# Kernel tuning notes

Measured on AMD Instinct MI355X. Metric: run time of the kernel, lower is better.

## Reference

```python
import jax, jax.numpy as jnp
import numpy as np
from jax import lax

S, B, K, T = 16, 16, 3, 20
FP, DP = 64, 28
CP = FP - DP + 1            # 37
P = CP * CP                 # 1369 == num_pixels
H, Hh, D = 256, 128, 2


def setup_inputs() -> dict:
    key = jax.random.key(0)
    ks = jax.random.split(key, 20)

    def lin_w(k, fan_in, fan_out):
        return jax.random.normal(k, (fan_in, fan_out), jnp.float32) / np.sqrt(fan_in)

    inp = {
        "frames": jax.random.uniform(ks[0], (B, T, FP, FP), jnp.float32),
        "digit": jax.random.uniform(ks[1], (S, B, K, DP, DP), jnp.float32),
        # enc_hidden: Linear(P, H)
        "w_h1": lin_w(ks[2], P, H), "b_h1": jnp.zeros((H,), jnp.float32),
        # where_mean: Linear(H, Hh) -> ReLU -> Linear(Hh, D) -> Tanh
        "wm1": lin_w(ks[3], H, Hh), "bm1": jnp.zeros((Hh,), jnp.float32),
        "wm2": lin_w(ks[4], Hh, D), "bm2": jnp.zeros((D,), jnp.float32),
        # where_log_std: Linear(H, Hh) -> ReLU -> Linear(Hh, D)
        "ws1": lin_w(ks[5], H, Hh), "bs1": jnp.zeros((Hh,), jnp.float32),
        "ws2": lin_w(ks[6], Hh, D), "bs2": jnp.zeros((D,), jnp.float32),
        # disp_mean: Linear(P, H) -> ReLU -> Linear(H, Hh) -> ReLU -> Linear(Hh, D) -> Tanh
        "wd1": lin_w(ks[7], P, H), "bd1": jnp.zeros((H,), jnp.float32),
        "wd2": lin_w(ks[8], H, Hh), "bd2": jnp.zeros((Hh,), jnp.float32),
        "wd3": lin_w(ks[9], Hh, D), "bd3": jnp.zeros((D,), jnp.float32),
    }
    return inp


def _lin(x, w, b):
    return x @ w + b


def _forward(frames, digit, w_h1, b_h1, wm1, bm1, wm2, bm2,
             ws1, bs1, ws2, bs2, wd1, bd1, wd2, bd2, wd3, bd3):
    # frames: (B, T, FP, FP); digit: (S, B, K, DP, DP)
    s, b, k_ = digit.shape[0], digit.shape[1], digit.shape[2]
    t = frames.shape[1]

    # Template correlation. The original builds a (T, S*B*K, FP, FP) repeated
    # input and runs conv2d with groups=S*B*K. Since frames do not depend on
    # (s, k), the identical math is a grouped conv with groups=B where group b
    # holds the S*K templates for batch element b.
    x = frames.transpose(1, 0, 2, 3)                          # (T, B, FP, FP)
    kern = digit.transpose(1, 0, 2, 3, 4).reshape(b * s * k_, 1, DP, DP)
    conv = lax.conv_general_dilated(
        x, kern, window_strides=(1, 1), padding='VALID',
        dimension_numbers=('NCHW', 'OIHW', 'NCHW'),
        feature_group_count=b)                                # (T, B*S*K, CP, CP)
    cp = conv.shape[-1]
    conv = conv.reshape(t, b, s, k_, cp * cp)
    conv = conv.transpose(2, 1, 0, 3, 4)                      # (S, B, T, K, P)

    # temporal displacement of correlation maps
    conv_disp = conv[:, :, 1:] - conv[:, :, :-1]              # (S, B, T-1, K, P)

    # disp_mean MLP
    d = jax.nn.relu(_lin(conv_disp, wd1, bd1))
    d = jax.nn.relu(_lin(d, wd2, bd2))
    disp = jnp.tanh(_lin(d, wd3, bd3))                        # (S, B, T-1, K, D)

    # enc_hidden on softmax-normalized correlation maps
    hidden = jax.nn.relu(_lin(jax.nn.softmax(conv, axis=-1), w_h1, b_h1))

    q_mean = jnp.tanh(_lin(jax.nn.relu(_lin(hidden, wm1, bm1)), wm2, bm2))
    q_std = jnp.exp(_lin(jax.nn.relu(_lin(hidden, ws1, bs1)), ws2, bs2))
    return q_mean, q_std, disp


def reference(frames, digit, w_h1, b_h1, wm1, bm1, wm2, bm2,
              ws1, bs1, ws2, bs2, wd1, bd1, wd2, bd2, wd3, bd3):
    return _forward(frames, digit, w_h1, b_h1, wm1, bm1, wm2, bm2,
                    ws1, bs1, ws2, bs2, wd1, bd1, wd2, bd2, wd3, bd3)
```

## Files before the change

### kernel.cpp

```cpp
#include <hip/hip_runtime.h>
#include <hip/hip_fp16.h>

typedef __attribute__((ext_vector_type(8))) _Float16 half8;
typedef __attribute__((ext_vector_type(2))) _Float16 h2f;
typedef __attribute__((ext_vector_type(4))) float f32x4;

#define NP 1369
#define KP 1376
#define NKT 43
#define ROWS_A 15360
#define ROWS_D 14592

#define PA_OFF   0
#define PD_OFF   (ROWS_A * KP)
#define PWH_OFF  (PD_OFF + ROWS_D * KP)
#define PWD_OFF  (PWH_OFF + NKT * 16 * 512)
#define PW2_OFF  (PWD_OFF + NKT * 16 * 512)
#define PWD2_OFF (PW2_OFF + 8 * 16 * 512)
#define TSUM_OFF (PWD2_OFF + 8 * 8 * 512)

#define SHIFT_DW 2384

__device__ __forceinline__ unsigned short f2h(float f) {
    __half h = __float2half(f);
    return __half_as_ushort(h);
}
__device__ __forceinline__ h2f u2h2(unsigned int u) {
    h2f r; __builtin_memcpy(&r, &u, 4); return r;
}

__global__ __launch_bounds__(256)
void k0_pack(const float* __restrict__ w_h1, const float* __restrict__ wd1,
             const float* __restrict__ wm1,  const float* __restrict__ ws1,
             const float* __restrict__ wd2,  const float* __restrict__ digit,
             unsigned short* __restrict__ wsu, float* __restrict__ tsum)
{
    const int tid = threadIdx.x;
    if (blockIdx.x >= 3136) {
        const int sbk = (blockIdx.x - 3136) * 4 + (tid >> 6);
        const int l = tid & 63;
        const float* tp = digit + (size_t)sbk * 784;
        float s = 0.f;
        for (int i = l; i < 784; i += 64) s += tp[i];
        for (int o = 32; o; o >>= 1) s += __shfl_xor(s, o, 64);
        if (l == 0) tsum[sbk] = 0.5f * s;
        return;
    }
    int idx = blockIdx.x * 256 + tid;
    int local, mode;
    unsigned short* dst;
    if (idx < 352256)      { mode = 0; local = idx;          dst = wsu + PWH_OFF; }
    else if (idx < 704512) { mode = 1; local = idx - 352256; dst = wsu + PWD_OFF; }
    else if (idx < 770048) { mode = 2; local = idx - 704512; dst = wsu + PW2_OFF; }
    else                   { mode = 3; local = idx - 770048; dst = wsu + PWD2_OFF; }
    int j = local & 7, lane = (local >> 3) & 63, rest = local >> 9;
    int NTn = (mode == 3) ? 8 : 16;
    int nt = rest % NTn, kt = rest / NTn;
    int k = kt * 32 + ((lane >> 4) << 3) + j;
    int n = nt * 16 + (lane & 15);
    float v = 0.f;
    if (mode == 0)      { if (k < NP) v = w_h1[k * 256 + n]; }
    else if (mode == 1) { if (k < NP) v = wd1[k * 256 + n]; }
    else if (mode == 2) { v = (n < 128) ? wm1[k * 128 + n] : ws1[k * 128 + (n - 128)]; }
    else                { v = wd2[k * 128 + n]; }
    dst[local] = f2h(v);
}

__global__ __launch_bounds__(512)
void k1a_corr(const float* __restrict__ frames, const float* __restrict__ digit,
              const float* __restrict__ tsum, unsigned short* __restrict__ wsu)
{
    __shared__ __align__(16) unsigned short Bs[7 * 3 * 512];
    __shared__ __align__(16) unsigned int frd[SHIFT_DW + 64 * 37];
    __shared__ float Cn[48];

    const int tid = threadIdx.x, l = tid & 63, w = tid >> 6;
    const int mh = blockIdx.x & 1;
    const int bt = blockIdx.x >> 1;
    const int t  = bt % 20;
    const int bb = bt / 20;

    if (tid < 48) {
        int sbk_n = ((tid / 3) * 16 + bb) * 3 + (tid % 3);
        Cn[tid] = tsum[sbk_n];
    }
    if (tid < 320) {
        int r = tid / 5, d2 = tid - r * 5;
        frd[r * 37 + 32 + d2] = 0u;
        frd[SHIFT_DW + r * 37 + 32 + d2] = 0u;
    }
    {
        const float4* fp4 = (const float4*)(frames + (size_t)(bb * 20 + t) * 4096);
        for (int idx = tid; idx < 1024; idx += 512) {
            float4 v = fp4[idx];
            int r = idx >> 4, c4 = idx & 15;
            unsigned lo = (unsigned)f2h(v.x) | ((unsigned)f2h(v.y) << 16);
            unsigned hi = (unsigned)f2h(v.z) | ((unsigned)f2h(v.w) << 16);
            frd[r * 37 + c4 * 2]     = lo;
            frd[r * 37 + c4 * 2 + 1] = hi;
        }
    }
    __syncthreads();
    for (int i = tid; i < 64 * 34; i += 512) {
        int r = i / 34, d = i - r * 34;
        unsigned lo = frd[r * 37 + d], hi = frd[r * 37 + d + 1];
        frd[SHIFT_DW + r * 37 + d] = (lo >> 16) | (hi << 16);
    }

    const int c15 = l & 15, quad = l >> 4, v0q = quad << 3;
    const int cnt = (50 - w) / 8;

    int baseb[6];
#pragma unroll
    for (int it = 0; it < 6; ++it) {
        int tI = mh * 43 + w + 8 * it;
        int p  = tI * 16 + c15;
        int pc = p > 1368 ? 1368 : p;
        int i  = pc / 37;
        int jj = pc - i * 37;
        int c  = jj + v0q;
        baseb[it] = (c & 1) * (SHIFT_DW * 4) + i * 148 + ((c >> 1) << 2);
    }
    f32x4 acc[6][3];
#pragma unroll
    for (int it = 0; it < 6; ++it)
#pragma unroll
        for (int nt = 0; nt < 3; ++nt) acc[it][nt] = (f32x4){0.f, 0.f, 0.f, 0.f};

    for (int ph = 0; ph < 4; ++ph) {
        __syncthreads();
        for (int s = tid; s < 1344; s += 512) {
            int ktl = s / 192;
            int rem = s - ktl * 192;
            int nt = rem >> 6, sl = rem & 63;
            int nl = nt * 16 + (sl & 15);
            int v0 = (sl >> 4) << 3;
            int kt = ph * 7 + ktl;
            int sbk_n = ((nl / 3) * 16 + bb) * 3 + (nl % 3);
            const float* tp = digit + (size_t)sbk_n * 784 + kt * 28 + v0;
            float4 fa = *(const float4*)tp;
            float4 fb = (v0 <= 16) ? *(const float4*)(tp + 4) : make_float4(0.f, 0.f, 0.f, 0.f);
            uint4 pk;
            pk.x = (unsigned)f2h(fa.x) | ((unsigned)f2h(fa.y) << 16);
            pk.y = (unsigned)f2h(fa.z) | ((unsigned)f2h(fa.w) << 16);
            pk.z = (unsigned)f2h(fb.x) | ((unsigned)f2h(fb.y) << 16);
            pk.w = (unsigned)f2h(fb.z) | ((unsigned)f2h(fb.w) << 16);
            *(uint4*)(Bs + s * 8) = pk;
        }
        __syncthreads();

        for (int ktl = 0; ktl < 7; ++ktl) {
            const int kt = ph * 7 + ktl;
            half8 bf0 = *(const half8*)(Bs + ktl * 1536 + 0 * 512 + l * 8);
            half8 bf1 = *(const half8*)(Bs + ktl * 1536 + 1 * 512 + l * 8);
            half8 bf2 = *(const half8*)(Bs + ktl * 1536 + 2 * 512 + l * 8);
            const char* fb2 = (const char*)frd + (size_t)kt * 148;
#pragma unroll
            for (int it = 0; it < 6; ++it) {
                if (it < cnt) {
                    const unsigned* ap = (const unsigned*)(fb2 + baseb[it]);
                    union { unsigned u[4]; half8 h8; } af;
                    af.u[0] = ap[0];
                    af.u[1] = ap[1];
                    af.u[2] = ap[2];
                    af.u[3] = ap[3];
                    acc[it][0] = __builtin_amdgcn_mfma_f32_16x16x32_f16(af.h8, bf0, acc[it][0], 0, 0, 0);
                    acc[it][1] = __builtin_amdgcn_mfma_f32_16x16x32_f16(af.h8, bf1, acc[it][1], 0, 0, 0);
                    acc[it][2] = __builtin_amdgcn_mfma_f32_16x16x32_f16(af.h8, bf2, acc[it][2], 0, 0, 0);
                }
            }
        }
    }

    for (int itg = 0; itg < 6; ++itg) {
        __syncthreads();
        if (itg < cnt) {
#pragma unroll
            for (int nt = 0; nt < 3; ++nt) {
                const int nl = nt * 16 + c15;
                const float C = Cn[nl];
                ushort4 st;
                st.x = f2h(acc[itg][nt][0] - C);
                st.y = f2h(acc[itg][nt][1] - C);
                st.z = f2h(acc[itg][nt][2] - C);
                st.w = f2h(acc[itg][nt][3] - C);
                *(ushort4*)(Bs + nl * 136 + w * 16 + quad * 4) = st;
            }
        }
        __syncthreads();
        const int nseg = (itg == 5) ? 6 : 16;
        for (int i = tid; i < 48 * nseg; i += 512) {
            int rowl = i / nseg, seg = i - rowl * nseg;
            int sbk_n = ((rowl / 3) * 16 + bb) * 3 + (rowl % 3);
            uint4 v = *(const uint4*)(Bs + rowl * 136 + seg * 8);
            *(uint4*)(wsu + PA_OFF + (size_t)(sbk_n * 20 + t) * KP
                      + mh * 688 + itg * 128 + seg * 8) = v;
        }
    }
}

__global__ __launch_bounds__(512)
void k2_gemmAB(unsigned short* __restrict__ wsu, const float* __restrict__ b_h1,
               const float* __restrict__ bm1, const float* __restrict__ bs1,
               const float* __restrict__ wm2, const float* __restrict__ bm2,
               const float* __restrict__ ws2, const float* __restrict__ bs2,
               float* __restrict__ out)
{
    __shared__ __align__(16) unsigned short Bbuf[2][2 * 8192];
    __shared__ __align__(16) unsigned short Hs[64 * 264];
    __shared__ float2 smstats[64];

    const int tid = threadIdx.x, l = tid & 63, w = tid >> 6;
    const int c15 = l & 15, quad = l >> 4;
    const int M0 = blockIdx.x * 64;
    unsigned short* Abase = wsu + PA_OFF;
    const unsigned short* PWH = wsu + PWH_OFF;
    const unsigned short* PWD = wsu + PWD_OFF;
    float* HR = (float*)(wsu + PD_OFF);

    const bool isH = (w < 4);
    const int wl = w & 3;
    const int row0 = M0 + wl * 16 + c15;
    const unsigned short* a0p = Abase + (size_t)row0 * KP + quad * 8;

    for (int rr = 0; rr < 8; ++rr) {
        const int lrow = w * 8 + rr;
        const unsigned* rp = (const unsigned*)(Abase + (size_t)(M0 + lrow) * KP);
        float f0[11], f1[11];
        float mx = -3.0e38f;
#pragma unroll
        for (int i = 0; i < 11; ++i) {
            int q = l + i * 64;
            unsigned u = (q < 685) ? rp[q] : 0u;
            h2f h = u2h2(u);
            f0[i] = (q < 685) ? (float)h[0] : -3.0e38f;
            f1[i] = (q < 684) ? (float)h[1] : -3.0e38f;
            mx = fmaxf(mx, fmaxf(f0[i], f1[i]));
        }
        for (int o = 32; o; o >>= 1) mx = fmaxf(mx, __shfl_xor(mx, o, 64));
        float sum = 0.f;
#pragma unroll
        for (int i = 0; i < 11; ++i)
            sum += __expf(f0[i] - mx) + __expf(f1[i] - mx);
        for (int o = 32; o; o >>= 1) sum += __shfl_xor(sum, o, 64);
        if (l == 0) smstats[lrow] = make_float2(mx, 1.0f / sum);
    }

    f32x4 acc[16];
#pragma unroll
    for (int n = 0; n < 16; ++n) acc[n] = (f32x4){0.f, 0.f, 0.f, 0.f};

    {
        const int4* sH = (const int4*)(PWH);
        const int4* sD = (const int4*)(PWD);
        int4* dH = (int4*)(Bbuf[0]);
        int4* dD = (int4*)(Bbuf[0] + 8192);
#pragma unroll
        for (int c = 0; c < 2; ++c) {
            dH[tid + 512 * c] = sH[tid + 512 * c];
            dD[tid + 512 * c] = sD[tid + 512 * c];
        }
    }
    half8 curA = *(const half8*)(a0p);
    __syncthreads();

    float2 st0 = make_float2(0.f, 0.f);
    if (isH) st0 = smstats[wl * 16 + c15];

    for (int kt = 0; kt < NKT; ++kt) {
        const int db = kt & 1;
        half8 nxtA = curA;
        if (kt + 1 < NKT) nxtA = *(const half8*)(a0p + (kt + 1) * 32);
        int4 rH[2], rD[2];
        if (kt + 1 < NKT) {
            const int4* sH = (const int4*)(PWH + (size_t)(kt + 1) * 8192);
            const int4* sD = (const int4*)(PWD + (size_t)(kt + 1) * 8192);
#pragma unroll
            for (int c = 0; c < 2; ++c) {
                rH[c] = sH[tid + 512 * c];
                rD[c] = sD[tid + 512 * c];
            }
        }
        half8 af = curA;
        if (isH) {
            union { half8 h8; unsigned u[4]; } ia, oa;
            ia.h8 = af;
#pragma unroll
            for (int q = 0; q < 4; ++q) {
                h2f ha = u2h2(ia.u[q]);
                float a0 = __expf((float)ha[0] - st0.x) * st0.y;
                float a1 = __expf((float)ha[1] - st0.x) * st0.y;
                oa.u[q] = (unsigned)f2h(a0) | ((unsigned)f2h(a1) << 16);
            }
            af = oa.h8;
        }
        const unsigned short* bb = Bbuf[db] + (isH ? 0 : 8192);
#pragma unroll
        for (int nt = 0; nt < 16; ++nt) {
            half8 bf = *(const half8*)(bb + nt * 512 + l * 8);
            acc[nt] = __builtin_amdgcn_mfma_f32_16x16x32_f16(af, bf, acc[nt], 0, 0, 0);
        }
        if (kt + 1 < NKT) {
            int4* dH = (int4*)(Bbuf[db ^ 1]);
            int4* dD = (int4*)(Bbuf[db ^ 1] + 8192);
#pragma unroll
            for (int c = 0; c < 2; ++c) {
                dH[tid + 512 * c] = rH[c];
                dD[tid + 512 * c] = rD[c];
            }
        }
        curA = nxtA;
        __syncthreads();
    }

    if (isH) {
#pragma unroll
        for (int nt = 0; nt < 16; ++nt) {
            const int col = nt * 16 + c15;
            const float bv = b_h1[col];
#pragma unroll
            for (int r = 0; r < 4; ++r) {
                const int lrow = wl * 16 + quad * 4 + r;
                const int csw = col ^ ((lrow & 7) << 3);
                float v = acc[nt][r] + bv;
                Hs[lrow * 264 + csw] = f2h(v > 0.f ? v : 0.f);
            }
        }
    } else {
#pragma unroll
        for (int nt = 0; nt < 16; ++nt) {
            const int col = nt * 16 + c15;
#pragma unroll
            for (int r = 0; r < 4; ++r) {
                const int row = M0 + wl * 16 + quad * 4 + r;
                HR[(size_t)row * 256 + col] = acc[nt][r];
            }
        }
    }
    __syncthreads();

    const unsigned short* PW2 = wsu + PW2_OFF;
    {
        const int4* src = (const int4*)(PW2);
        int4* dst = (int4*)(Bbuf[0]);
#pragma unroll
        for (int cc = 0; cc < 2; ++cc) dst[tid + 512 * cc] = src[tid + 512 * cc];
    }
    __syncthreads();

    f32x4 acc2[16];
#pragma unroll
    for (int n = 0; n < 16; ++n) acc2[n] = (f32x4){0.f, 0.f, 0.f, 0.f};

    const int hr0 = wl * 16 + c15;
    for (int kt = 0; kt < 8; ++kt) {
        const int db = kt & 1;
        int4 rB2[2];
        if (kt + 1 < 8) {
            const int4* src = (const int4*)(PW2 + (size_t)(kt + 1) * 8192);
#pragma unroll
            for (int cc = 0; cc < 2; ++cc) rB2[cc] = src[tid + 512 * cc];
        }
        if (isH) {
            const int hoff = (kt * 32 + quad * 8) ^ ((hr0 & 7) << 3);
            half8 af2 = *(const half8*)(Hs + hr0 * 264 + hoff);
#pragma unroll
            for (int nt = 0; nt < 16; ++nt) {
                half8 bf = *(const half8*)(Bbuf[db] + nt * 512 + l * 8);
                acc2[nt] = __builtin_amdgcn_mfma_f32_16x16x32_f16(af2, bf, acc2[nt], 0, 0, 0);
            }
        }
        if (kt + 1 < 8) {
            int4* dst = (int4*)(Bbuf[db ^ 1]);
#pragma unroll
            for (int cc = 0; cc < 2; ++cc) dst[tid + 512 * cc] = rB2[cc];
        }
        __syncthreads();
    }

    if (isH) {
#pragma unroll
        for (int nt = 0; nt < 16; ++nt) {
            float bv = (nt < 8) ? bm1[nt * 16 + c15] : bs1[(nt - 8) * 16 + c15];
#pragma unroll
            for (int r = 0; r < 4; ++r) {
                float v = acc2[nt][r] + bv;
                acc2[nt][r] = v > 0.f ? v : 0.f;
            }
        }
        float pm[2][4], ps[2][4];
#pragma unroll
        for (int d = 0; d < 2; ++d)
#pragma unroll
            for (int r = 0; r < 4; ++r) { pm[d][r] = 0.f; ps[d][r] = 0.f; }
#pragma unroll
        for (int d = 0; d < 2; ++d)
#pragma unroll
            for (int nt = 0; nt < 8; ++nt) {
                const float wmv = wm2[(nt * 16 + c15) * 2 + d];
                const float wsv = ws2[(nt * 16 + c15) * 2 + d];
#pragma unroll
                for (int r = 0; r < 4; ++r) {
                    pm[d][r] = fmaf(acc2[nt][r], wmv, pm[d][r]);
                    ps[d][r] = fmaf(acc2[nt + 8][r], wsv, ps[d][r]);
                }
            }
#pragma unroll
        for (int o = 1; o < 16; o <<= 1)
#pragma unroll
            for (int d = 0; d < 2; ++d)
#pragma unroll
                for (int r = 0; r < 4; ++r) {
                    pm[d][r] += __shfl_xor(pm[d][r], o, 64);
                    ps[d][r] += __shfl_xor(ps[d][r], o, 64);
                }
        if (c15 == 0) {
#pragma unroll
            for (int r = 0; r < 4; ++r) {
                const int orow = M0 + wl * 16 + quad * 4 + r;
                const int sbk = orow / 20, t = orow % 20;
                const int sb = sbk / 3, kk = sbk % 3;
                const int oi = ((sb * 20 + t) * 3 + kk) * 2;
                out[oi + 0] = tanhf(pm[0][r] + bm2[0]);
                out[oi + 1] = tanhf(pm[1][r] + bm2[1]);
                out[30720 + oi + 0] = __expf(ps[0][r] + bs2[0]);
                out[30720 + oi + 1] = __expf(ps[1][r] + bs2[1]);
            }
        }
    }
}

template <bool PATHA>
__global__ __launch_bounds__(256)
void k2_heads(unsigned short* __restrict__ wsu,
              const float* __restrict__ b1a, const float* __restrict__ b1b,
              const float* __restrict__ w2a, const float* __restrict__ b2a,
              const float* __restrict__ w2b, const float* __restrict__ b2b,
              const float* __restrict__ bd1, float* __restrict__ out)
{
    constexpr int NT2 = PATHA ? 16 : 8;
    constexpr int NI4 = NT2 / 4;
    __shared__ __align__(16) unsigned short Bsh[2][NT2 * 512];
    const int tid = threadIdx.x, l = tid & 63, w = tid >> 6;
    const int c = l & 15, quad = l >> 4;
    const int M0 = blockIdx.x * 64;
    const unsigned short* PW = wsu + (PATHA ? PW2_OFF : PWD2_OFF);

    f32x4 acc[NT2];
#pragma unroll
    for (int n = 0; n < NT2; ++n) acc[n] = (f32x4){0.f, 0.f, 0.f, 0.f};

    const int row = M0 + w * 16 + c;
    const unsigned short* arow = nullptr;
    const float* h1p = nullptr; const float* h0p = nullptr;
    if (PATHA) {
        arow = wsu + PA_OFF + (size_t)row * KP + quad * 8;
    } else {
        const float* HR = (const float*)(wsu + PD_OFF);
        const int sbk = row / 19, dt = row % 19;
        h0p = HR + (size_t)(sbk * 20 + dt) * 256 + quad * 8;
        h1p = h0p + 256;
    }

    {
        const int4* src = (const int4*)(PW);
        int4* dst = (int4*)Bsh[0];
#pragma unroll
        for (int cc = 0; cc < NI4; ++cc)
            dst[tid + 256 * cc] = src[tid + 256 * cc];
    }
    half8 curPA = {};
    float4 c1a = {}, c1b = {}, c0a = {}, c0b = {};
    if (PATHA) {
        curPA = *(const half8*)(arow);
    } else {
        c1a = *(const float4*)(h1p); c1b = *(const float4*)(h1p + 4);
        c0a = *(const float4*)(h0p); c0b = *(const float4*)(h0p + 4);
    }
    __syncthreads();

    for (int kt = 0; kt < 8; ++kt) {
        const int db = kt & 1;
        half8 nxtPA = curPA;
        float4 n1a = c1a, n1b = c1b, n0a = c0a, n0b = c0b;
        if (kt + 1 < 8) {
            if (PATHA) {
                nxtPA = *(const half8*)(arow + (kt + 1) * 32);
            } else {
                n1a = *(const float4*)(h1p + (kt + 1) * 32);
                n1b = *(const float4*)(h1p + (kt + 1) * 32 + 4);
                n0a = *(const float4*)(h0p + (kt + 1) * 32);
                n0b = *(const float4*)(h0p + (kt + 1) * 32 + 4);
            }
        }
        int4 rB[NI4];
        if (kt + 1 < 8) {
            const int4* src = (const int4*)(PW + (size_t)(kt + 1) * (NT2 * 512));
#pragma unroll
            for (int cc = 0; cc < NI4; ++cc) rB[cc] = src[tid + 256 * cc];
        }
        half8 af;
        if (PATHA) {
            af = curPA;
        } else {
            float4 bb = *(const float4*)(bd1 + kt * 32 + quad * 8);
            float4 bb2 = *(const float4*)(bd1 + kt * 32 + quad * 8 + 4);
            float v0 = fmaxf(c1a.x - c0a.x + bb.x, 0.f);
            float v1 = fmaxf(c1a.y - c0a.y + bb.y, 0.f);
            float v2 = fmaxf(c1a.z - c0a.z + bb.z, 0.f);
            float v3 = fmaxf(c1a.w - c0a.w + bb.w, 0.f);
            float v4 = fmaxf(c1b.x - c0b.x + bb2.x, 0.f);
            float v5 = fmaxf(c1b.y - c0b.y + bb2.y, 0.f);
            float v6 = fmaxf(c1b.z - c0b.z + bb2.z, 0.f);
            float v7 = fmaxf(c1b.w - c0b.w + bb2.w, 0.f);
            union { unsigned u[4]; half8 h8; } pk;
            pk.u[0] = (unsigned)f2h(v0) | ((unsigned)f2h(v1) << 16);
            pk.u[1] = (unsigned)f2h(v2) | ((unsigned)f2h(v3) << 16);
            pk.u[2] = (unsigned)f2h(v4) | ((unsigned)f2h(v5) << 16);
            pk.u[3] = (unsigned)f2h(v6) | ((unsigned)f2h(v7) << 16);
            af = pk.h8;
        }
#pragma unroll
        for (int nt = 0; nt < NT2; ++nt) {
            half8 bf = *(const half8*)(Bsh[db] + nt * 512 + l * 8);
            acc[nt] = __builtin_amdgcn_mfma_f32_16x16x32_f16(af, bf, acc[nt], 0, 0, 0);
        }
        if (kt + 1 < 8) {
            int4* dst = (int4*)Bsh[db ^ 1];
#pragma unroll
            for (int cc = 0; cc < NI4; ++cc) dst[tid + 256 * cc] = rB[cc];
        }
        curPA = nxtPA;
        c1a = n1a; c1b = n1b; c0a = n0a; c0b = n0b;
        __syncthreads();
    }
#pragma unroll
    for (int nt = 0; nt < NT2; ++nt) {
        float bv;
        if (PATHA) bv = (nt < 8) ? b1a[nt * 16 + c] : b1b[(nt - 8) * 16 + c];
        else       bv = b1a[nt * 16 + c];
#pragma unroll
        for (int r = 0; r < 4; ++r) {
            float v = acc[nt][r] + bv;
            acc[nt][r] = v > 0.f ? v : 0.f;
        }
    }
    float pm[2][4], ps[2][4];
#pragma unroll
    for (int d = 0; d < 2; ++d)
#pragma unroll
        for (int r = 0; r < 4; ++r) { pm[d][r] = 0.f; ps[d][r] = 0.f; }
#pragma unroll
    for (int d = 0; d < 2; ++d)
#pragma unroll
        for (int nt = 0; nt < 8; ++nt) {
            const float wmv = w2a[(nt * 16 + c) * 2 + d];
            float wsv = 0.f;
            if (PATHA) wsv = w2b[(nt * 16 + c) * 2 + d];
#pragma unroll
            for (int r = 0; r < 4; ++r) {
                pm[d][r] = fmaf(acc[nt][r], wmv, pm[d][r]);
                if (PATHA) ps[d][r] = fmaf(acc[nt + 8][r], wsv, ps[d][r]);
            }
        }
#pragma unroll
    for (int o = 1; o < 16; o <<= 1)
#pragma unroll
        for (int d = 0; d < 2; ++d)
#pragma unroll
            for (int r = 0; r < 4; ++r) {
                pm[d][r] += __shfl_xor(pm[d][r], o, 64);
                if (PATHA) ps[d][r] += __shfl_xor(ps[d][r], o, 64);
            }
    if (c == 0) {
#pragma unroll
        for (int r = 0; r < 4; ++r) {
            const int orow = M0 + w * 16 + quad * 4 + r;
            if (PATHA) {
                const int sbk = orow / 20, t = orow % 20;
                const int sb = sbk / 3, kk = sbk % 3;
                const int oi = ((sb * 20 + t) * 3 + kk) * 2;
                out[oi + 0] = tanhf(pm[0][r] + b2a[0]);
                out[oi + 1] = tanhf(pm[1][r] + b2a[1]);
                out[30720 + oi + 0] = __expf(ps[0][r] + b2b[0]);
                out[30720 + oi + 1] = __expf(ps[1][r] + b2b[1]);
            } else {
                const int sbk = orow / 19, dt = orow % 19;
                const int sb = sbk / 3, kk = sbk % 3;
                const int oi = 61440 + ((sb * 19 + dt) * 3 + kk) * 2;
                out[oi + 0] = tanhf(pm[0][r] + b2a[0]);
                out[oi + 1] = tanhf(pm[1][r] + b2a[1]);
            }
        }
    }
}

extern "C" void kernel_launch(void* const* d_in, const int* in_sizes, int n_in,
                              void* d_out, int out_size, void* d_ws, size_t ws_size,
                              hipStream_t stream) {
    const float* frames = (const float*)d_in[0];
    const float* digit  = (const float*)d_in[1];
    const float* w_h1   = (const float*)d_in[2];
    const float* b_h1   = (const float*)d_in[3];
    const float* wm1    = (const float*)d_in[4];
    const float* bm1    = (const float*)d_in[5];
    const float* wm2    = (const float*)d_in[6];
    const float* bm2    = (const float*)d_in[7];
    const float* ws1    = (const float*)d_in[8];
    const float* bs1    = (const float*)d_in[9];
    const float* ws2    = (const float*)d_in[10];
    const float* bs2    = (const float*)d_in[11];
    const float* wd1    = (const float*)d_in[12];
    const float* bd1    = (const float*)d_in[13];
    const float* wd2    = (const float*)d_in[14];
    const float* bd2    = (const float*)d_in[15];
    const float* wd3    = (const float*)d_in[16];
    const float* bd3    = (const float*)d_in[17];

    unsigned short* wsu = (unsigned short*)d_ws;
    float* tsum = (float*)(wsu + TSUM_OFF);
    float* o = (float*)d_out;

    k0_pack<<<dim3(3328), dim3(256), 0, stream>>>(w_h1, wd1, wm1, ws1, wd2, digit, wsu, tsum);
    k1a_corr<<<dim3(640), dim3(512), 0, stream>>>(frames, digit, tsum, wsu);
    k2_gemmAB<<<dim3(240), dim3(512), 0, stream>>>(wsu, b_h1, bm1, bs1, wm2, bm2, ws2, bs2, o);
    k2_heads<false><<<dim3(228), dim3(256), 0, stream>>>(wsu, bd2, nullptr, wd3, bd3, nullptr, nullptr, bd1, o);
}
```

Before: 126.7 us.

## Split H and D GEMM paths into separate blocks and prepack digit templates

The fused GEMM kernel used to run the hidden-path and displacement-path waves inside one 512-thread block. It is now a 256-thread kernel launched with twice as many blocks, each block doing only one path, so more blocks can spread across the CUs. In exchange, each block loads its full B tile by itself, and displacement blocks exit early after writing results. Separately, the pack kernel now converts the digit templates to fp16 once, in a padded layout, so the correlation kernel loads packed uint4 values instead of converting fp32 in every block. This adds one extra pass over the templates.

```diff
diff --git a/kernel.cpp b/kernel.cpp
--- a/kernel.cpp
+++ b/kernel.cpp
@@ -36,6 +36,22 @@
              unsigned short* __restrict__ wsu, float* __restrict__ tsum)
 {
     const int tid = threadIdx.x;
+    if (blockIdx.x >= 3328) {
+        int g = (blockIdx.x - 3328) * 256 + tid;
+        int sbk = g / 112;
+        int rem = g - sbk * 112;
+        int kt = rem >> 2, v0g = rem & 3;
+        const float* tp = digit + (size_t)sbk * 784 + kt * 28 + v0g * 8;
+        float4 fa = *(const float4*)tp;
+        float4 fb = (v0g < 3) ? *(const float4*)(tp + 4) : make_float4(0.f, 0.f, 0.f, 0.f);
+        uint4 pk;
+        pk.x = (unsigned)f2h(fa.x) | ((unsigned)f2h(fa.y) << 16);
+        pk.y = (unsigned)f2h(fa.z) | ((unsigned)f2h(fa.w) << 16);
+        pk.z = (unsigned)f2h(fb.x) | ((unsigned)f2h(fb.y) << 16);
+        pk.w = (unsigned)f2h(fb.z) | ((unsigned)f2h(fb.w) << 16);
+        *(uint4*)(wsu + PD_OFF + (size_t)g * 8) = pk;
+        return;
+    }
     if (blockIdx.x >= 3136) {
         const int sbk = (blockIdx.x - 3136) * 4 + (tid >> 6);
         const int l = tid & 63;
@@ -79,6 +95,7 @@
     const int bt = blockIdx.x >> 1;
     const int t  = bt % 20;
     const int bb = bt / 20;
+    const unsigned short* pdig = wsu + PD_OFF;
 
     if (tid < 48) {
         int sbk_n = ((tid / 3) * 16 + bb) * 3 + (tid % 3);
@@ -134,17 +151,9 @@
             int rem = s - ktl * 192;
             int nt = rem >> 6, sl = rem & 63;
             int nl = nt * 16 + (sl & 15);
-            int v0 = (sl >> 4) << 3;
             int kt = ph * 7 + ktl;
             int sbk_n = ((nl / 3) * 16 + bb) * 3 + (nl % 3);
-            const float* tp = digit + (size_t)sbk_n * 784 + kt * 28 + v0;
-            float4 fa = *(const float4*)tp;
-            float4 fb = (v0 <= 16) ? *(const float4*)(tp + 4) : make_float4(0.f, 0.f, 0.f, 0.f);
-            uint4 pk;
-            pk.x = (unsigned)f2h(fa.x) | ((unsigned)f2h(fa.y) << 16);
-            pk.y = (unsigned)f2h(fa.z) | ((unsigned)f2h(fa.w) << 16);
-            pk.z = (unsigned)f2h(fb.x) | ((unsigned)f2h(fb.y) << 16);
-            pk.w = (unsigned)f2h(fb.z) | ((unsigned)f2h(fb.w) << 16);
+            uint4 pk = *(const uint4*)(pdig + (size_t)sbk_n * 896 + kt * 32 + (sl >> 4) * 8);
             *(uint4*)(Bs + s * 8) = pk;
         }
         __syncthreads();
@@ -199,51 +208,51 @@
     }
 }
 
-__global__ __launch_bounds__(512)
-void k2_gemmAB(unsigned short* __restrict__ wsu, const float* __restrict__ b_h1,
-               const float* __restrict__ bm1, const float* __restrict__ bs1,
-               const float* __restrict__ wm2, const float* __restrict__ bm2,
-               const float* __restrict__ ws2, const float* __restrict__ bs2,
-               float* __restrict__ out)
+__global__ __launch_bounds__(256)
+void k2_gemm(unsigned short* __restrict__ wsu, const float* __restrict__ b_h1,
+             const float* __restrict__ bm1, const float* __restrict__ bs1,
+             const float* __restrict__ wm2, const float* __restrict__ bm2,
+             const float* __restrict__ ws2, const float* __restrict__ bs2,
+             float* __restrict__ out)
 {
-    __shared__ __align__(16) unsigned short Bbuf[2][2 * 8192];
+    __shared__ __align__(16) unsigned short Bbuf[2][8192];
     __shared__ __align__(16) unsigned short Hs[64 * 264];
     __shared__ float2 smstats[64];
 
     const int tid = threadIdx.x, l = tid & 63, w = tid >> 6;
     const int c15 = l & 15, quad = l >> 4;
-    const int M0 = blockIdx.x * 64;
+    const bool isH = (blockIdx.x < 240);
+    const int M0 = (isH ? blockIdx.x : blockIdx.x - 240) * 64;
     unsigned short* Abase = wsu + PA_OFF;
-    const unsigned short* PWH = wsu + PWH_OFF;
-    const unsigned short* PWD = wsu + PWD_OFF;
+    const unsigned short* PW1 = wsu + (isH ? PWH_OFF : PWD_OFF);
     float* HR = (float*)(wsu + PD_OFF);
 
-    const bool isH = (w < 4);
-    const int wl = w & 3;
-    const int row0 = M0 + wl * 16 + c15;
+    const int row0 = M0 + w * 16 + c15;
     const unsigned short* a0p = Abase + (size_t)row0 * KP + quad * 8;
 
-    for (int rr = 0; rr < 8; ++rr) {
-        const int lrow = w * 8 + rr;
-        const unsigned* rp = (const unsigned*)(Abase + (size_t)(M0 + lrow) * KP);
-        float f0[11], f1[11];
-        float mx = -3.0e38f;
-#pragma unroll
-        for (int i = 0; i < 11; ++i) {
-            int q = l + i * 64;
-            unsigned u = (q < 685) ? rp[q] : 0u;
-            h2f h = u2h2(u);
-            f0[i] = (q < 685) ? (float)h[0] : -3.0e38f;
-            f1[i] = (q < 684) ? (float)h[1] : -3.0e38f;
-            mx = fmaxf(mx, fmaxf(f0[i], f1[i]));
-        }
-        for (int o = 32; o; o >>= 1) mx = fmaxf(mx, __shfl_xor(mx, o, 64));
-        float sum = 0.f;
-#pragma unroll
-        for (int i = 0; i < 11; ++i)
-            sum += __expf(f0[i] - mx) + __expf(f1[i] - mx);
-        for (int o = 32; o; o >>= 1) sum += __shfl_xor(sum, o, 64);
-        if (l == 0) smstats[lrow] = make_float2(mx, 1.0f / sum);
+    if (isH) {
+        for (int rr = 0; rr < 16; ++rr) {
+            const int lrow = w * 16 + rr;
+            const unsigned* rp = (const unsigned*)(Abase + (size_t)(M0 + lrow) * KP);
+            float f0[11], f1[11];
+            float mx = -3.0e38f;
+#pragma unroll
+            for (int i = 0; i < 11; ++i) {
+                int q = l + i * 64;
+                unsigned u = (q < 685) ? rp[q] : 0u;
+                h2f h = u2h2(u);
+                f0[i] = (q < 685) ? (float)h[0] : -3.0e38f;
+                f1[i] = (q < 684) ? (float)h[1] : -3.0e38f;
+                mx = fmaxf(mx, fmaxf(f0[i], f1[i]));
+            }
+            for (int o = 32; o; o >>= 1) mx = fmaxf(mx, __shfl_xor(mx, o, 64));
+            float sum = 0.f;
+#pragma unroll
+            for (int i = 0; i < 11; ++i)
+                sum += __expf(f0[i] - mx) + __expf(f1[i] - mx);
+            for (int o = 32; o; o >>= 1) sum += __shfl_xor(sum, o, 64);
+            if (l == 0) smstats[lrow] = make_float2(mx, 1.0f / sum);
+        }
     }
 
     f32x4 acc[16];
@@ -251,35 +260,26 @@
     for (int n = 0; n < 16; ++n) acc[n] = (f32x4){0.f, 0.f, 0.f, 0.f};
 
     {
-        const int4* sH = (const int4*)(PWH);
-        const int4* sD = (const int4*)(PWD);
-        int4* dH = (int4*)(Bbuf[0]);
-        int4* dD = (int4*)(Bbuf[0] + 8192);
-#pragma unroll
-        for (int c = 0; c < 2; ++c) {
-            dH[tid + 512 * c] = sH[tid + 512 * c];
-            dD[tid + 512 * c] = sD[tid + 512 * c];
-        }
+        const int4* src = (const int4*)(PW1);
+        int4* dst = (int4*)(Bbuf[0]);
+#pragma unroll
+        for (int c = 0; c < 4; ++c) dst[tid + 256 * c] = src[tid + 256 * c];
     }
     half8 curA = *(const half8*)(a0p);
     __syncthreads();
 
     float2 st0 = make_float2(0.f, 0.f);
-    if (isH) st0 = smstats[wl * 16 + c15];
+    if (isH) st0 = smstats[w * 16 + c15];
 
     for (int kt = 0; kt < NKT; ++kt) {
         const int db = kt & 1;
         half8 nxtA = curA;
         if (kt + 1 < NKT) nxtA = *(const half8*)(a0p + (kt + 1) * 32);
-        int4 rH[2], rD[2];
+        int4 rB[4];
         if (kt + 1 < NKT) {
-            const int4* sH = (const int4*)(PWH + (size_t)(kt + 1) * 8192);
-            const int4* sD = (const int4*)(PWD + (size_t)(kt + 1) * 8192);
-#pragma unroll
-            for (int c = 0; c < 2; ++c) {
-                rH[c] = sH[tid + 512 * c];
-                rD[c] = sD[tid + 512 * c];
-            }
+            const int4* src = (const int4*)(PW1 + (size_t)(kt + 1) * 8192);
+#pragma unroll
+            for (int c = 0; c < 4; ++c) rB[c] = src[tid + 256 * c];
         }
         half8 af = curA;
         if (isH) {
@@ -294,47 +294,43 @@
             }
             af = oa.h8;
         }
-        const unsigned short* bb = Bbuf[db] + (isH ? 0 : 8192);
 #pragma unroll
         for (int nt = 0; nt < 16; ++nt) {
-            half8 bf = *(const half8*)(bb + nt * 512 + l * 8);
+            half8 bf = *(const half8*)(Bbuf[db] + nt * 512 + l * 8);
             acc[nt] = __builtin_amdgcn_mfma_f32_16x16x32_f16(af, bf, acc[nt], 0, 0, 0);
         }
         if (kt + 1 < NKT) {
-            int4* dH = (int4*)(Bbuf[db ^ 1]);
-            int4* dD = (int4*)(Bbuf[db ^ 1] + 8192);
-#pragma unroll
-            for (int c = 0; c < 2; ++c) {
-                dH[tid + 512 * c] = rH[c];
-                dD[tid + 512 * c] = rD[c];
-            }
+            int4* dst = (int4*)(Bbuf[db ^ 1]);
+#pragma unroll
+            for (int c = 0; c < 4; ++c) dst[tid + 256 * c] = rB[c];
         }
         curA = nxtA;
         __syncthreads();
     }
 
-    if (isH) {
+    if (!isH) {
 #pragma unroll
         for (int nt = 0; nt < 16; ++nt) {
             const int col = nt * 16 + c15;
-            const float bv = b_h1[col];
 #pragma unroll
             for (int r = 0; r < 4; ++r) {
-                const int lrow = wl * 16 + quad * 4 + r;
-                const int csw = col ^ ((lrow & 7) << 3);
-                float v = acc[nt][r] + bv;
-                Hs[lrow * 264 + csw] = f2h(v > 0.f ? v : 0.f);
-            }
-        }
-    } else {
-#pragma unroll
-        for (int nt = 0; nt < 16; ++nt) {
-            const int col = nt * 16 + c15;
-#pragma unroll
-            for (int r = 0; r < 4; ++r) {
-                const int row = M0 + wl * 16 + quad * 4 + r;
+                const int row = M0 + w * 16 + quad * 4 + r;
                 HR[(size_t)row * 256 + col] = acc[nt][r];
             }
+        }
+        return;
+    }
+
+#pragma unroll
+    for (int nt = 0; nt < 16; ++nt) {
+        const int col = nt * 16 + c15;
+        const float bv = b_h1[col];
+#pragma unroll
+        for (int r = 0; r < 4; ++r) {
+            const int lrow = w * 16 + quad * 4 + r;
+            const int csw = col ^ ((lrow & 7) << 3);
+            float v = acc[nt][r] + bv;
+            Hs[lrow * 264 + csw] = f2h(v > 0.f ? v : 0.f);
         }
     }
     __syncthreads();
@@ -344,7 +340,7 @@
         const int4* src = (const int4*)(PW2);
         int4* dst = (int4*)(Bbuf[0]);
 #pragma unroll
-        for (int cc = 0; cc < 2; ++cc) dst[tid + 512 * cc] = src[tid + 512 * cc];
+        for (int cc = 0; cc < 4; ++cc) dst[tid + 256 * cc] = src[tid + 256 * cc];
     }
     __syncthreads();
 
@@ -352,16 +348,16 @@
 #pragma unroll
     for (int n = 0; n < 16; ++n) acc2[n] = (f32x4){0.f, 0.f, 0.f, 0.f};
 
-    const int hr0 = wl * 16 + c15;
+    const int hr0 = w * 16 + c15;
     for (int kt = 0; kt < 8; ++kt) {
         const int db = kt & 1;
-        int4 rB2[2];
+        int4 rB2[4];
         if (kt + 1 < 8) {
             const int4* src = (const int4*)(PW2 + (size_t)(kt + 1) * 8192);
 #pragma unroll
-            for (int cc = 0; cc < 2; ++cc) rB2[cc] = src[tid + 512 * cc];
-        }
-        if (isH) {
+            for (int cc = 0; cc < 4; ++cc) rB2[cc] = src[tid + 256 * cc];
+        }
+        {
             const int hoff = (kt * 32 + quad * 8) ^ ((hr0 & 7) << 3);
             half8 af2 = *(const half8*)(Hs + hr0 * 264 + hoff);
 #pragma unroll
@@ -373,12 +369,12 @@
         if (kt + 1 < 8) {
             int4* dst = (int4*)(Bbuf[db ^ 1]);
 #pragma unroll
-            for (int cc = 0; cc < 2; ++cc) dst[tid + 512 * cc] = rB2[cc];
+            for (int cc = 0; cc < 4; ++cc) dst[tid + 256 * cc] = rB2[cc];
         }
         __syncthreads();
     }
 
-    if (isH) {
+    {
 #pragma unroll
         for (int nt = 0; nt < 16; ++nt) {
             float bv = (nt < 8) ? bm1[nt * 16 + c15] : bs1[(nt - 8) * 16 + c15];
@@ -417,7 +413,7 @@
         if (c15 == 0) {
 #pragma unroll
             for (int r = 0; r < 4; ++r) {
-                const int orow = M0 + wl * 16 + quad * 4 + r;
+                const int orow = M0 + w * 16 + quad * 4 + r;
                 const int sbk = orow / 20, t = orow % 20;
                 const int sb = sbk / 3, kk = sbk % 3;
                 const int oi = ((sb * 20 + t) * 3 + kk) * 2;
@@ -621,8 +617,8 @@
     float* tsum = (float*)(wsu + TSUM_OFF);
     float* o = (float*)d_out;
 
-    k0_pack<<<dim3(3328), dim3(256), 0, stream>>>(w_h1, wd1, wm1, ws1, wd2, digit, wsu, tsum);
+    k0_pack<<<dim3(3664), dim3(256), 0, stream>>>(w_h1, wd1, wm1, ws1, wd2, digit, wsu, tsum);
     k1a_corr<<<dim3(640), dim3(512), 0, stream>>>(frames, digit, tsum, wsu);
-    k2_gemmAB<<<dim3(240), dim3(512), 0, stream>>>(wsu, b_h1, bm1, bs1, wm2, bm2, ws2, bs2, o);
+    k2_gemm<<<dim3(480), dim3(256), 0, stream>>>(wsu, b_h1, bm1, bs1, wm2, bm2, ws2, bs2, o);
     k2_heads<false><<<dim3(228), dim3(256), 0, stream>>>(wsu, bd2, nullptr, wd3, bd3, nullptr, nullptr, bd1, o);
 }
```

Result: no change. 128.4 us (+1.4%).
